# Kernel tuning notes

Measured on AMD Instinct MI355X. Metric: run time of the kernel, lower is better.

Reference implementation:

```python
import jax, jax.numpy as jnp
import numpy as np

B, S, H = 16, 8192, 256

def setup_inputs() -> dict:
    key = jax.random.key(0)
    k1, k2, k3, k4, k5 = jax.random.split(key, 5)
    scale = 1.0 / np.sqrt(H)
    return {
        "hidden": jax.random.normal(k1, (B, H), dtype=jnp.float32),
        "encoder_outputs": jax.random.normal(k2, (B, S, H), dtype=jnp.float32),
        "W1": jax.random.uniform(k3, (H, H), dtype=jnp.float32, minval=-scale, maxval=scale),
        "W2": jax.random.uniform(k4, (H, H), dtype=jnp.float32, minval=-scale, maxval=scale),
        "V": jax.random.uniform(k5, (1, H), dtype=jnp.float32, minval=-scale, maxval=scale),
    }

def reference(hidden, encoder_outputs, W1, W2, V):
    # hidden: [B, H], encoder_outputs: [B, S, H]
    h1 = jnp.einsum('bh,kh->bk', hidden, W1)[:, None, :]        # [B, 1, H]
    h2 = jnp.einsum('bsh,kh->bsk', encoder_outputs, W2)          # [B, S, H]
    scores = jnp.einsum('bsh,oh->bso', jnp.tanh(h1 + h2), V)     # [B, S, 1]
    attn = jax.nn.softmax(scores, axis=1)                        # softmax over seq dim
    context = jnp.sum(attn * encoder_outputs, axis=1)            # [B, H]
    # torch: unsqueeze/transpose/repeat/squeeze/permute -> tile context over seq: [B, H, S]
    context_tiled = jnp.broadcast_to(context[:, :, None], (context.shape[0], context.shape[1], encoder_outputs.shape[1]))
    return (context_tiled, context, attn[:, :, 0])
```

## Files before the change

### kernel.cpp

```cpp
#include <hip/hip_runtime.h>
#include <hip/hip_bf16.h>
#include <math.h>

#define B_ 16
#define S_ 8192
#define H_ 256
#define NBLK 32
#define TILE_R 32
#define T_PER_BLK 8
#define LROW 264

using bf16x8 = __attribute__((ext_vector_type(8))) short;
using f32x4 = __attribute__((ext_vector_type(4))) float;

__device__ inline short f2bf(float x) {
  union {
    float f;
    unsigned u;
  } v;
  v.f = x;
  unsigned r = v.u + 0x7FFFu + ((v.u >> 16) & 1u);
  return (short)(r >> 16);
}

__device__ inline bf16x8 pack8(float4 a, float4 b) {
  union {
    __hip_bfloat162 h[4];
    bf16x8 v;
  } u;
  u.h[0] = __float22bfloat162_rn(make_float2(a.x, a.y));
  u.h[1] = __float22bfloat162_rn(make_float2(a.z, a.w));
  u.h[2] = __float22bfloat162_rn(make_float2(b.x, b.y));
  u.h[3] = __float22bfloat162_rn(make_float2(b.z, b.w));
  return u.v;
}

__device__ inline float fast_tanh(float x) {
  float e = exp2f(x * 2.885390082f);
  return fmaf(-2.f, __builtin_amdgcn_rcpf(e + 1.f), 1.f);
}

__global__ __launch_bounds__(256) void prep_kernel(
    const float* __restrict__ hidden, const float* __restrict__ W1,
    const float* __restrict__ W2, short* __restrict__ W2f,
    float* __restrict__ h1) {
  const int blk = blockIdx.x;
  const int t = threadIdx.x;
  if (blk < 32) {
    const int gid = blk * 256 + t;
    const int l = gid & 63;
    const int j0 = (gid >> 6) & 15;
    const int ks = gid >> 10;
    const int row = j0 * 16 + (l & 15);
    const int col = ks * 32 + (l >> 4) * 8;
    const float* wp = W2 + row * H_ + col;
    bf16x8 out;
#pragma unroll
    for (int i = 0; i < 8; ++i) out[i] = f2bf(wp[i]);
    *(bf16x8*)(W2f + (size_t)gid * 8) = out;
  } else {
    const int b = blk - 32;
    const float* hrow = hidden + b * H_;
    const float* wrow = W1 + t * H_;
    float acc = 0.f;
#pragma unroll 8
    for (int h = 0; h < H_; ++h) acc += hrow[h] * wrow[h];
    h1[b * H_ + t] = acc;
  }
}

__global__ __launch_bounds__(512, 4) void scores_ctx_kernel(
    const float* __restrict__ enc, const short* __restrict__ W2f,
    const float* __restrict__ h1, const float* __restrict__ V,
    float* __restrict__ expsc, float* __restrict__ c_blk,
    float* __restrict__ l_blk) {
  __shared__ __align__(16) short albuf[2][TILE_R * LROW];
  __shared__ float pcomb[8][33];
  __shared__ float avec[TILE_R];
  __shared__ float2 clds2[4][129];

  const int tid = threadIdx.x;
  const int w = tid >> 6;
  const int l = tid & 63;
  const int lo = l & 15;
  const int hi = l >> 4;
  const int bid = blockIdx.x;
  const int b = bid >> 5;
  const int blk = bid & 31;
  const int s_base = blk * (TILE_R * T_PER_BLK);

  const bf16x8* bbase = (const bf16x8*)W2f;
  bf16x8 bfrag[8][2];
#pragma unroll
  for (int ks = 0; ks < 8; ++ks)
#pragma unroll
    for (int jj = 0; jj < 2; ++jj)
      bfrag[ks][jj] = bbase[(ks * 16 + (2 * w + jj)) * 64 + l];

  float h1v[2], Vv[2];
#pragma unroll
  for (int jj = 0; jj < 2; ++jj) {
    h1v[jj] = h1[b * H_ + (2 * w + jj) * 16 + lo];
    Vv[jj] = V[(2 * w + jj) * 16 + lo];
  }

  const int r0 = tid >> 5;
  const int kc0 = tid & 31;
  const float4* gsrc = (const float4*)(enc + (size_t)b * S_ * H_);

  const int rg = tid >> 7;
  const int cp = tid & 127;
  float c0 = 0.f, c1 = 0.f, l_part = 0.f;

  {
    size_t gi0 = ((size_t)(s_base + r0) * (H_ / 4)) + kc0 * 2;
    size_t gi1 = ((size_t)(s_base + r0 + 16) * (H_ / 4)) + kc0 * 2;
    float4 a0 = gsrc[gi0], a1 = gsrc[gi0 + 1];
    float4 b0 = gsrc[gi1], b1 = gsrc[gi1 + 1];
    *(bf16x8*)&albuf[0][r0 * LROW + kc0 * 8] = pack8(a0, a1);
    *(bf16x8*)&albuf[0][(r0 + 16) * LROW + kc0 * 8] = pack8(b0, b1);
  }
  __syncthreads();

  const int b0s = lo & 1;
  const int b1s = (lo >> 1) & 1;
  const int b2s = (lo >> 2) & 1;

  for (int t = 0; t < T_PER_BLK; ++t) {
    const int cur = t & 1;

    float4 na0, na1, nb0, nb1;
    if (t + 1 < T_PER_BLK) {
      size_t gi0 =
          ((size_t)(s_base + (t + 1) * TILE_R + r0) * (H_ / 4)) + kc0 * 2;
      size_t gi1 =
          ((size_t)(s_base + (t + 1) * TILE_R + r0 + 16) * (H_ / 4)) + kc0 * 2;
      na0 = gsrc[gi0];
      na1 = gsrc[gi0 + 1];
      nb0 = gsrc[gi1];
      nb1 = gsrc[gi1 + 1];
    }

    f32x4 acc[2][2];
#pragma unroll
    for (int m = 0; m < 2; ++m)
#pragma unroll
      for (int jj = 0; jj < 2; ++jj) acc[m][jj] = (f32x4){0.f, 0.f, 0.f, 0.f};

    const short* abase = &albuf[cur][lo * LROW + hi * 8];
#pragma unroll
    for (int ks = 0; ks < 8; ++ks) {
      bf16x8 a0 = *(const bf16x8*)(abase + ks * 32);
      bf16x8 a1 = *(const bf16x8*)(abase + 16 * LROW + ks * 32);
      acc[0][0] = __builtin_amdgcn_mfma_f32_16x16x32_bf16(a0, bfrag[ks][0], acc[0][0], 0, 0, 0);
      acc[0][1] = __builtin_amdgcn_mfma_f32_16x16x32_bf16(a0, bfrag[ks][1], acc[0][1], 0, 0, 0);
      acc[1][0] = __builtin_amdgcn_mfma_f32_16x16x32_bf16(a1, bfrag[ks][0], acc[1][0], 0, 0, 0);
      acc[1][1] = __builtin_amdgcn_mfma_f32_16x16x32_bf16(a1, bfrag[ks][1], acc[1][1], 0, 0, 0);
    }

    float p0 = fast_tanh(acc[0][0][0] + h1v[0]) * Vv[0] + fast_tanh(acc[0][1][0] + h1v[1]) * Vv[1];
    float p1 = fast_tanh(acc[0][0][1] + h1v[0]) * Vv[0] + fast_tanh(acc[0][1][1] + h1v[1]) * Vv[1];
    float p2 = fast_tanh(acc[0][0][2] + h1v[0]) * Vv[0] + fast_tanh(acc[0][1][2] + h1v[1]) * Vv[1];
    float p3 = fast_tanh(acc[0][0][3] + h1v[0]) * Vv[0] + fast_tanh(acc[0][1][3] + h1v[1]) * Vv[1];
    float p4 = fast_tanh(acc[1][0][0] + h1v[0]) * Vv[0] + fast_tanh(acc[1][1][0] + h1v[1]) * Vv[1];
    float p5 = fast_tanh(acc[1][0][1] + h1v[0]) * Vv[0] + fast_tanh(acc[1][1][1] + h1v[1]) * Vv[1];
    float p6 = fast_tanh(acc[1][0][2] + h1v[0]) * Vv[0] + fast_tanh(acc[1][1][2] + h1v[1]) * Vv[1];
    float p7 = fast_tanh(acc[1][0][3] + h1v[0]) * Vv[0] + fast_tanh(acc[1][1][3] + h1v[1]) * Vv[1];

    float q0 = (b0s ? p1 : p0) + __shfl_xor((b0s ? p0 : p1), 1, 16);
    float q1 = (b0s ? p3 : p2) + __shfl_xor((b0s ? p2 : p3), 1, 16);
    float q2 = (b0s ? p5 : p4) + __shfl_xor((b0s ? p4 : p5), 1, 16);
    float q3 = (b0s ? p7 : p6) + __shfl_xor((b0s ? p6 : p7), 1, 16);
    float r0q = (b1s ? q1 : q0) + __shfl_xor((b1s ? q0 : q1), 2, 16);
    float r1q = (b1s ? q3 : q2) + __shfl_xor((b1s ? q2 : q3), 2, 16);
    float u = (b2s ? r1q : r0q) + __shfl_xor((b2s ? r0q : r1q), 4, 16);
    u += __shfl_xor(u, 8, 16);

    if (lo < 8) {
      const int row = ((lo >> 2) & 1) * 16 + hi * 4 + (lo & 3);
      pcomb[w][row] = u;
    }
    __syncthreads();

    if (tid < TILE_R) {
      float s = 0.f;
#pragma unroll
      for (int ww = 0; ww < 8; ++ww) s += pcomb[ww][tid];
      float e = exp2f(s * 1.44269504f);
      avec[tid] = e;
      expsc[(size_t)b * S_ + s_base + t * TILE_R + tid] = e;
      l_part += e;
    }
    __syncthreads();

    const unsigned* ab32 = (const unsigned*)&albuf[cur][0];
#pragma unroll
    for (int k = 0; k < 8; ++k) {
      const int r = rg * 8 + k;
      unsigned vb = ab32[r * 132 + cp];
      float a = avec[r];
      float he = __uint_as_float(vb << 16);
      float ho = __uint_as_float(vb & 0xFFFF0000u);
      c0 = fmaf(a, he, c0);
      c1 = fmaf(a, ho, c1);
    }

    if (t + 1 < T_PER_BLK) {
      *(bf16x8*)&albuf[cur ^ 1][r0 * LROW + kc0 * 8] = pack8(na0, na1);
      *(bf16x8*)&albuf[cur ^ 1][(r0 + 16) * LROW + kc0 * 8] = pack8(nb0, nb1);
    }
    __syncthreads();
  }

  clds2[rg][cp] = make_float2(c0, c1);
  __syncthreads();
  if (tid < 128) {
    float2 s0 = clds2[0][tid], s1 = clds2[1][tid];
    float2 s2 = clds2[2][tid], s3 = clds2[3][tid];
    float2 r;
    r.x = s0.x + s1.x + s2.x + s3.x;
    r.y = s0.y + s1.y + s2.y + s3.y;
    ((float2*)(c_blk + ((size_t)(b * NBLK + blk)) * H_))[tid] = r;
  }
  if (w == 0) {
    float lp = l_part;
#pragma unroll
    for (int off = 32; off > 0; off >>= 1) lp += __shfl_xor(lp, off, 64);
    if (l == 0) l_blk[b * NBLK + blk] = lp;
  }
}

__global__ __launch_bounds__(256) void attn_norm_kernel(
    const float* __restrict__ expsc, const float* __restrict__ l_blk,
    float* __restrict__ out2) {
  const int b = blockIdx.y;
  const int tid = threadIdx.x;
  float lg = 0.f;
#pragma unroll
  for (int j = 0; j < NBLK; ++j) lg += l_blk[b * NBLK + j];
  const float inv = 1.f / lg;
  const size_t base = (size_t)b * S_ + blockIdx.x * 2048;
  const float4* ip = (const float4*)(expsc + base);
  float4* op = (float4*)(out2 + base);
  float4 x0 = ip[tid * 2];
  float4 x1 = ip[tid * 2 + 1];
  float4 y0 = {x0.x * inv, x0.y * inv, x0.z * inv, x0.w * inv};
  float4 y1 = {x1.x * inv, x1.y * inv, x1.z * inv, x1.w * inv};
  op[tid * 2] = y0;
  op[tid * 2 + 1] = y1;
}

__global__ __launch_bounds__(256) void ctx_tile_kernel(
    const float* __restrict__ c_blk, const float* __restrict__ l_blk,
    float* __restrict__ out0, float* __restrict__ out1) {
  const int h = blockIdx.x;
  const int b = blockIdx.y;
  const int tid = threadIdx.x;
  float lg = 0.f;
#pragma unroll
  for (int j = 0; j < NBLK; ++j) lg += l_blk[b * NBLK + j];
  float cs = 0.f;
#pragma unroll
  for (int j = 0; j < NBLK; ++j)
    cs += c_blk[((size_t)(b * NBLK + j)) * H_ + h];
  const float ctx = cs / lg;
  if (tid == 0) out1[b * H_ + h] = ctx;
  float4 vv = {ctx, ctx, ctx, ctx};
  float4* op = (float4*)(out0 + ((size_t)b * H_ + h) * S_);
#pragma unroll 4
  for (int i = tid; i < S_ / 4; i += 256) op[i] = vv;
}

extern "C" void kernel_launch(void* const* d_in, const int* in_sizes, int n_in,
                              void* d_out, int out_size, void* d_ws,
                              size_t ws_size, hipStream_t stream) {
  const float* hidden = (const float*)d_in[0];
  const float* enc = (const float*)d_in[1];
  const float* W1 = (const float*)d_in[2];
  const float* W2 = (const float*)d_in[3];
  const float* V = (const float*)d_in[4];

  float* out0 = (float*)d_out;
  float* out1 = out0 + (size_t)B_ * H_ * S_;
  float* out2 = out1 + B_ * H_;

  float* ws = (float*)d_ws;
  short* W2f = (short*)ws;
  float* h1 = ws + 32768;
  float* expsc = h1 + B_ * H_;
  float* l_blk = expsc + (size_t)B_ * S_;
  float* c_blk = l_blk + B_ * NBLK;

  prep_kernel<<<48, 256, 0, stream>>>(hidden, W1, W2, W2f, h1);
  scores_ctx_kernel<<<B_ * NBLK, 512, 0, stream>>>(enc, W2f, h1, V, expsc,
                                                   c_blk, l_blk);
  attn_norm_kernel<<<dim3(4, B_), 256, 0, stream>>>(expsc, l_blk, out2);
  ctx_tile_kernel<<<dim3(H_, B_), 256, 0, stream>>>(c_blk, l_blk, out0, out1);
}
```

Before: 78.64 us.

## Drop per-tile barrier, spread exp across waves, merge finishing kernels

Moves the prefetch write into the next LDS buffer ahead of the exp stage, which removes one __syncthreads per tile iteration. The 32 exp computations are now spread across all 8 waves (4 lanes each) instead of one wave, and the l_part sum goes through a small shared-memory reduction. The attention-normalize and context-tile kernels become a single launch that uses blockIdx.x to pick its role, saving one kernel launch. The buffer-hazard reasoning is subtler, and the merged kernel mixes uneven block workloads.

Result: faster. 76.67 us (-2.5%).

```diff
diff --git a/kernel.cpp b/kernel.cpp
--- a/kernel.cpp
+++ b/kernel.cpp
@@ -78,6 +78,7 @@
   __shared__ float pcomb[8][33];
   __shared__ float avec[TILE_R];
   __shared__ float2 clds2[4][129];
+  __shared__ float lsum[8];
 
   const int tid = threadIdx.x;
   const int w = tid >> 6;
@@ -182,13 +183,19 @@
     }
     __syncthreads();
 
-    if (tid < TILE_R) {
+    if (t + 1 < T_PER_BLK) {
+      *(bf16x8*)&albuf[cur ^ 1][r0 * LROW + kc0 * 8] = pack8(na0, na1);
+      *(bf16x8*)&albuf[cur ^ 1][(r0 + 16) * LROW + kc0 * 8] = pack8(nb0, nb1);
+    }
+
+    if (l < 4) {
+      const int row = w * 4 + l;
       float s = 0.f;
 #pragma unroll
-      for (int ww = 0; ww < 8; ++ww) s += pcomb[ww][tid];
+      for (int ww = 0; ww < 8; ++ww) s += pcomb[ww][row];
       float e = exp2f(s * 1.44269504f);
-      avec[tid] = e;
-      expsc[(size_t)b * S_ + s_base + t * TILE_R + tid] = e;
+      avec[row] = e;
+      expsc[(size_t)b * S_ + s_base + t * TILE_R + row] = e;
       l_part += e;
     }
     __syncthreads();
@@ -204,14 +211,12 @@
       c0 = fmaf(a, he, c0);
       c1 = fmaf(a, ho, c1);
     }
-
-    if (t + 1 < T_PER_BLK) {
-      *(bf16x8*)&albuf[cur ^ 1][r0 * LROW + kc0 * 8] = pack8(na0, na1);
-      *(bf16x8*)&albuf[cur ^ 1][(r0 + 16) * LROW + kc0 * 8] = pack8(nb0, nb1);
-    }
-    __syncthreads();
-  }
-
+  }
+
+  float lp = l_part;
+  lp += __shfl_xor(lp, 1);
+  lp += __shfl_xor(lp, 2);
+  if (l == 0) lsum[w] = lp;
   clds2[rg][cp] = make_float2(c0, c1);
   __syncthreads();
   if (tid < 128) {
@@ -222,53 +227,49 @@
     r.y = s0.y + s1.y + s2.y + s3.y;
     ((float2*)(c_blk + ((size_t)(b * NBLK + blk)) * H_))[tid] = r;
   }
-  if (w == 0) {
-    float lp = l_part;
-#pragma unroll
-    for (int off = 32; off > 0; off >>= 1) lp += __shfl_xor(lp, off, 64);
-    if (l == 0) l_blk[b * NBLK + blk] = lp;
-  }
-}
-
-__global__ __launch_bounds__(256) void attn_norm_kernel(
+  if (tid == 0) {
+    float ls = 0.f;
+#pragma unroll
+    for (int ww = 0; ww < 8; ++ww) ls += lsum[ww];
+    l_blk[b * NBLK + blk] = ls;
+  }
+}
+
+__global__ __launch_bounds__(256) void finish_kernel(
     const float* __restrict__ expsc, const float* __restrict__ l_blk,
-    float* __restrict__ out2) {
+    const float* __restrict__ c_blk, float* __restrict__ out0,
+    float* __restrict__ out1, float* __restrict__ out2) {
+  const int bx = blockIdx.x;
   const int b = blockIdx.y;
   const int tid = threadIdx.x;
   float lg = 0.f;
 #pragma unroll
   for (int j = 0; j < NBLK; ++j) lg += l_blk[b * NBLK + j];
   const float inv = 1.f / lg;
-  const size_t base = (size_t)b * S_ + blockIdx.x * 2048;
-  const float4* ip = (const float4*)(expsc + base);
-  float4* op = (float4*)(out2 + base);
-  float4 x0 = ip[tid * 2];
-  float4 x1 = ip[tid * 2 + 1];
-  float4 y0 = {x0.x * inv, x0.y * inv, x0.z * inv, x0.w * inv};
-  float4 y1 = {x1.x * inv, x1.y * inv, x1.z * inv, x1.w * inv};
-  op[tid * 2] = y0;
-  op[tid * 2 + 1] = y1;
-}
-
-__global__ __launch_bounds__(256) void ctx_tile_kernel(
-    const float* __restrict__ c_blk, const float* __restrict__ l_blk,
-    float* __restrict__ out0, float* __restrict__ out1) {
-  const int h = blockIdx.x;
-  const int b = blockIdx.y;
-  const int tid = threadIdx.x;
-  float lg = 0.f;
-#pragma unroll
-  for (int j = 0; j < NBLK; ++j) lg += l_blk[b * NBLK + j];
-  float cs = 0.f;
-#pragma unroll
-  for (int j = 0; j < NBLK; ++j)
-    cs += c_blk[((size_t)(b * NBLK + j)) * H_ + h];
-  const float ctx = cs / lg;
-  if (tid == 0) out1[b * H_ + h] = ctx;
-  float4 vv = {ctx, ctx, ctx, ctx};
-  float4* op = (float4*)(out0 + ((size_t)b * H_ + h) * S_);
+
+  if (bx < 4) {
+    const size_t base = (size_t)b * S_ + bx * 2048;
+    const float4* ip = (const float4*)(expsc + base);
+    float4* op = (float4*)(out2 + base);
+    float4 x0 = ip[tid * 2];
+    float4 x1 = ip[tid * 2 + 1];
+    float4 y0 = {x0.x * inv, x0.y * inv, x0.z * inv, x0.w * inv};
+    float4 y1 = {x1.x * inv, x1.y * inv, x1.z * inv, x1.w * inv};
+    op[tid * 2] = y0;
+    op[tid * 2 + 1] = y1;
+  } else {
+    const int h = bx - 4;
+    float cs = 0.f;
+#pragma unroll
+    for (int j = 0; j < NBLK; ++j)
+      cs += c_blk[((size_t)(b * NBLK + j)) * H_ + h];
+    const float ctx = cs * inv;
+    if (tid == 0) out1[b * H_ + h] = ctx;
+    float4 vv = {ctx, ctx, ctx, ctx};
+    float4* op = (float4*)(out0 + ((size_t)b * H_ + h) * S_);
 #pragma unroll 4
-  for (int i = tid; i < S_ / 4; i += 256) op[i] = vv;
+    for (int i = tid; i < S_ / 4; i += 256) op[i] = vv;
+  }
 }
 
 extern "C" void kernel_launch(void* const* d_in, const int* in_sizes, int n_in,
@@ -294,6 +295,6 @@
   prep_kernel<<<48, 256, 0, stream>>>(hidden, W1, W2, W2f, h1);
   scores_ctx_kernel<<<B_ * NBLK, 512, 0, stream>>>(enc, W2f, h1, V, expsc,
                                                    c_blk, l_blk);
-  attn_norm_kernel<<<dim3(4, B_), 256, 0, stream>>>(expsc, l_blk, out2);
-  ctx_tile_kernel<<<dim3(H_, B_), 256, 0, stream>>>(c_blk, l_blk, out0, out1);
-}
+  finish_kernel<<<dim3(H_ + 4, B_), 256, 0, stream>>>(expsc, l_blk, c_blk,
+                                                      out0, out1, out2);
+}
```
